# Kernel tuning notes

Measured on AMD Instinct MI355X. Metric: run time of the kernel, lower is better.

Reference implementation:

```python
import jax, jax.numpy as jnp
import numpy as np

B, T, D, U = 2, 512, 768, 768


def setup_inputs() -> dict:
    key = jax.random.key(0)
    kx, kv, ku, kw = jax.random.split(key, 4)
    x = jax.random.normal(kx, (B, T, D), dtype=jnp.float32)
    # glorot-ish scaled params
    V_a = jax.random.normal(kv, (U,), dtype=jnp.float32) * (1.0 / np.sqrt(U))
    U_a = jax.random.normal(ku, (D, U), dtype=jnp.float32) * (1.0 / np.sqrt(D))
    b_u = jnp.zeros((U,), dtype=jnp.float32)
    W_a = jax.random.normal(kw, (D, U), dtype=jnp.float32) * (1.0 / np.sqrt(D))
    return {"x": x, "V_a": V_a, "U_a": U_a, "b_u": b_u, "W_a": W_a}


def reference(x, V_a, U_a, b_u, W_a):
    # Bahdanau additive self-attention, fully batched (replaces the per-timestep loop).
    # wx[b,i,u] = x[b,i] @ W_a  (query projection; original recomputed this per step)
    wx = jnp.einsum('bid,du->biu', x, W_a)
    # ux[b,j,u] = x[b,j] @ U_a + b_u  (the _uxpb term)
    ux = jnp.einsum('bjd,du->bju', x, U_a) + b_u
    # e[b,i,j] = V_a . tanh(wx[b,i] + ux[b,j])
    e = jnp.einsum('biju,u->bij', jnp.tanh(wx[:, :, None, :] + ux[:, None, :, :]), V_a)
    # original: exp / sum over keys == softmax over axis j (no mask path)
    at = jax.nn.softmax(e, axis=2)
    # context[b,i,d] = sum_j at[b,i,j] * x[b,j,d]
    return jnp.einsum('bij,bjd->bid', at, x)
```

## Files before the change

### kernel.cpp

```cpp
#include <hip/hip_runtime.h>
#include <hip/hip_bf16.h>

#define BB 2
#define TT 512
#define DD 768
#define UU 768
#define NR (BB*TT)
#define CC 2.8853900817779268f

typedef __attribute__((ext_vector_type(8))) short short8v;
typedef __attribute__((ext_vector_type(4))) float float4v;
typedef __attribute__((ext_vector_type(4))) unsigned short ushort4v;

static __device__ __forceinline__ float fexp2(float x) { return __builtin_amdgcn_exp2f(x); }
static __device__ __forceinline__ float frcp(float x)  { return __builtin_amdgcn_rcpf(x); }
static __device__ __forceinline__ float readlane_f(float v, int l) {
    return __builtin_bit_cast(float, __builtin_amdgcn_readlane(__builtin_bit_cast(unsigned, v), l));
}
static __device__ __forceinline__ unsigned short bf16rn(float f) {
    unsigned u = __builtin_bit_cast(unsigned, f);
    u += 0x7FFFu + ((u >> 16) & 1u);
    return (unsigned short)(u >> 16);
}
static __device__ __forceinline__ float bf16tof(unsigned short h) {
    return __builtin_bit_cast(float, ((unsigned)h) << 16);
}

__global__ __launch_bounds__(256) void prep_split(
    const float* __restrict__ x,
    const float* __restrict__ Wm,
    const float* __restrict__ Um,
    unsigned short* __restrict__ xhi, unsigned short* __restrict__ xlo,
    unsigned short* __restrict__ WThi, unsigned short* __restrict__ WTlo,
    unsigned short* __restrict__ UThi, unsigned short* __restrict__ UTlo)
{
    const int mode = blockIdx.z;
    const int t = threadIdx.x;

    if (mode == 2) {
        const int blk = blockIdx.y * 12 + blockIdx.x;
        const float4* src = (const float4*)x + (size_t)blk * 1024;
        #pragma unroll
        for (int i = 0; i < 4; ++i) {
            const int idx = i * 256 + t;
            const float4 v = src[idx];
            ushort4v h, l;
            h.x = bf16rn(v.x); l.x = bf16rn(v.x - bf16tof(h.x));
            h.y = bf16rn(v.y); l.y = bf16rn(v.y - bf16tof(h.y));
            h.z = bf16rn(v.z); l.z = bf16rn(v.z - bf16tof(h.z));
            h.w = bf16rn(v.w); l.w = bf16rn(v.w - bf16tof(h.w));
            const size_t off = (size_t)blk * 4096 + (size_t)idx * 4;
            *(ushort4v*)(xhi + off) = h;
            *(ushort4v*)(xlo + off) = l;
        }
        return;
    }
    if (blockIdx.y >= 12) return;

    const float* __restrict__ S = (mode == 0) ? Wm : Um;
    unsigned short* __restrict__ Thi = (mode == 0) ? WThi : UThi;
    unsigned short* __restrict__ Tlo = (mode == 0) ? WTlo : UTlo;

    __shared__ float tile[64][65];
    const int d0 = blockIdx.y * 64;
    const int u0 = blockIdx.x * 64;

    #pragma unroll
    for (int i = 0; i < 4; ++i) {
        const int f4 = i * 256 + t;
        const int r  = f4 >> 4;
        const int c4 = f4 & 15;
        const float4 v = *(const float4*)(S + (size_t)(d0 + r) * UU + u0 + c4 * 4);
        tile[r][c4 * 4 + 0] = v.x;
        tile[r][c4 * 4 + 1] = v.y;
        tile[r][c4 * 4 + 2] = v.z;
        tile[r][c4 * 4 + 3] = v.w;
    }
    __syncthreads();
    #pragma unroll
    for (int i = 0; i < 2; ++i) {
        const int cid = i * 256 + t;
        const int ur  = cid >> 3;
        const int kc  = cid & 7;
        short8v H, L;
        #pragma unroll
        for (int j = 0; j < 8; ++j) {
            const float f = tile[kc * 8 + j][ur];
            const unsigned short h = bf16rn(f);
            H[j] = (short)h;
            L[j] = (short)bf16rn(f - bf16tof(h));
        }
        const size_t off = (size_t)(u0 + ur) * DD + d0 + kc * 8;
        *(short8v*)(Thi + off) = H;
        *(short8v*)(Tlo + off) = L;
    }
}

__global__ __launch_bounds__(256) void gemm_mfma(
    const unsigned short* __restrict__ xhi, const unsigned short* __restrict__ xlo,
    const unsigned short* __restrict__ WThi, const unsigned short* __restrict__ WTlo,
    const unsigned short* __restrict__ UThi, const unsigned short* __restrict__ UTlo,
    const float* __restrict__ bu,
    float* __restrict__ EW4,
    float* __restrict__ EUT)
{
    const int mode = blockIdx.z;
    const unsigned short* __restrict__ Ahi = mode ? UThi : WThi;
    const unsigned short* __restrict__ Alo = mode ? UTlo : WTlo;

    __shared__ unsigned short lds[4 * 4096];

    const int tid  = threadIdx.x;
    const int lane = tid & 63;
    const int wid  = tid >> 6;
    const int wm   = wid >> 1, wn = wid & 1;
    const int u0   = blockIdx.y * 64;
    const int r0t  = blockIdx.x * 64;

    const int srow0 = tid >> 3;
    const int srow1 = srow0 + 32;
    const int sc0   = tid & 7;
    const int sw0   = (sc0 ^ (srow0 & 7)) << 3;

    short8v g0, g1, g2, g3, g4, g5, g6, g7;

#define LOADSTEP(K0) { \
    const size_t ka = (size_t)(K0) + sc0 * 8; \
    g0 = *(const short8v*)(Ahi + (size_t)(u0 + srow0) * DD + ka); \
    g1 = *(const short8v*)(Ahi + (size_t)(u0 + srow1) * DD + ka); \
    g2 = *(const short8v*)(Alo + (size_t)(u0 + srow0) * DD + ka); \
    g3 = *(const short8v*)(Alo + (size_t)(u0 + srow1) * DD + ka); \
    g4 = *(const short8v*)(xhi + (size_t)(r0t + srow0) * DD + ka); \
    g5 = *(const short8v*)(xhi + (size_t)(r0t + srow1) * DD + ka); \
    g6 = *(const short8v*)(xlo + (size_t)(r0t + srow0) * DD + ka); \
    g7 = *(const short8v*)(xlo + (size_t)(r0t + srow1) * DD + ka); }

#define WRITESTEP { \
    *(short8v*)&lds[0 * 4096 + srow0 * 64 + sw0] = g0; \
    *(short8v*)&lds[0 * 4096 + srow1 * 64 + sw0] = g1; \
    *(short8v*)&lds[1 * 4096 + srow0 * 64 + sw0] = g2; \
    *(short8v*)&lds[1 * 4096 + srow1 * 64 + sw0] = g3; \
    *(short8v*)&lds[2 * 4096 + srow0 * 64 + sw0] = g4; \
    *(short8v*)&lds[2 * 4096 + srow1 * 64 + sw0] = g5; \
    *(short8v*)&lds[3 * 4096 + srow0 * 64 + sw0] = g6; \
    *(short8v*)&lds[3 * 4096 + srow1 * 64 + sw0] = g7; }

    float4v acc[2][2] = {};

    LOADSTEP(0);
    for (int s = 0; s < 12; ++s) {
        __syncthreads();
        WRITESTEP;
        __syncthreads();
        if (s < 11) LOADSTEP((s + 1) * 64);

        short8v ah[2][2], al[2][2], bh[2][2], bl[2][2];
        #pragma unroll
        for (int f = 0; f < 2; ++f) {
            const int arow = wm * 32 + f * 16 + (lane & 15);
            const int brow = wn * 32 + f * 16 + (lane & 15);
            #pragma unroll
            for (int kk = 0; kk < 2; ++kk) {
                const int ck = kk * 4 + (lane >> 4);
                ah[f][kk] = *(const short8v*)&lds[0 * 4096 + arow * 64 + (((ck ^ (arow & 7))) << 3)];
                al[f][kk] = *(const short8v*)&lds[1 * 4096 + arow * 64 + (((ck ^ (arow & 7))) << 3)];
                bh[f][kk] = *(const short8v*)&lds[2 * 4096 + brow * 64 + (((ck ^ (brow & 7))) << 3)];
                bl[f][kk] = *(const short8v*)&lds[3 * 4096 + brow * 64 + (((ck ^ (brow & 7))) << 3)];
            }
        }
        #pragma unroll
        for (int kk = 0; kk < 2; ++kk)
            #pragma unroll
            for (int m = 0; m < 2; ++m)
                #pragma unroll
                for (int n = 0; n < 2; ++n) {
                    acc[m][n] = __builtin_amdgcn_mfma_f32_16x16x32_bf16(ah[m][kk], bh[n][kk], acc[m][n], 0, 0, 0);
                    acc[m][n] = __builtin_amdgcn_mfma_f32_16x16x32_bf16(ah[m][kk], bl[n][kk], acc[m][n], 0, 0, 0);
                    acc[m][n] = __builtin_amdgcn_mfma_f32_16x16x32_bf16(al[m][kk], bh[n][kk], acc[m][n], 0, 0, 0);
                }
    }

    #pragma unroll
    for (int m = 0; m < 2; ++m) {
        #pragma unroll
        for (int n = 0; n < 2; ++n) {
            const int ub = u0 + wm * 32 + m * 16 + ((lane >> 4) << 2);
            const int r  = r0t + wn * 32 + n * 16 + (lane & 15);
            if (mode == 0) {
                float* dst = EW4 + ((size_t)(r >> 2) * UU + ub) * 4 + (r & 3);
                #pragma unroll
                for (int reg = 0; reg < 4; ++reg)
                    dst[reg * 4] = fexp2(acc[m][n][reg] * CC);
            } else {
                const int b = r >> 9, j = r & 511;
                const float4 bv = *(const float4*)(bu + ub);
                float4v o;
                o[0] = fexp2((acc[m][n][0] + bv.x) * CC);
                o[1] = fexp2((acc[m][n][1] + bv.y) * CC);
                o[2] = fexp2((acc[m][n][2] + bv.z) * CC);
                o[3] = fexp2((acc[m][n][3] + bv.w) * CC);
                *(float4v*)(EUT + (size_t)b * (UU * TT) + (size_t)(ub >> 2) * (TT * 4) + j * 4) = o;
            }
        }
    }
#undef LOADSTEP
#undef WRITESTEP
}

__global__ __launch_bounds__(512) void attn_fused(
    const float* __restrict__ x,
    const float* __restrict__ V_a,
    const float* __restrict__ EW4,
    const float* __restrict__ EUT,
    float* __restrict__ out)
{
    extern __shared__ float smem[];
    float*  part = smem;
    float*  red  = smem;
    float4* sw4  = (float4*)(smem + 12288);
    float*  vv   = smem + 12288 + 3072;

    const int tid  = threadIdx.x;
    const int lane = tid & 63;
    const int w    = tid >> 6;

    const int bid = blockIdx.x;
    const int blk = (bid & 7) * 32 + (bid >> 3);

    const int r0 = blk * 4;
    const int b  = r0 >> 9;

    {
        const float4* __restrict__ ew4q = (const float4*)EW4 + (size_t)blk * UU;
        for (int t = tid; t < UU; t += 512) {
            sw4[t] = ew4q[t];
            vv[t]  = V_a[t];
        }
    }
    __syncthreads();

    const float4* __restrict__ eq = (const float4*)(EUT + (size_t)b * UU * TT) + tid;

    float acc0 = 0.f, acc1 = 0.f, acc2 = 0.f, acc3 = 0.f;

#define PAIR(E0, E1, u0) { \
    const float4 S0 = sw4[(u0)]; \
    const float4 S1 = sw4[(u0) + 1]; \
    const float v0 = vv[(u0)], v1 = vv[(u0) + 1]; \
    { const float da = fmaf((E0), S0.x, 1.f), db = fmaf((E1), S1.x, 1.f); \
      float n = v0 * db; n = fmaf(v1, da, n); \
      acc0 = fmaf(n, frcp(da * db), acc0); } \
    { const float da = fmaf((E0), S0.y, 1.f), db = fmaf((E1), S1.y, 1.f); \
      float n = v0 * db; n = fmaf(v1, da, n); \
      acc1 = fmaf(n, frcp(da * db), acc1); } \
    { const float da = fmaf((E0), S0.z, 1.f), db = fmaf((E1), S1.z, 1.f); \
      float n = v0 * db; n = fmaf(v1, da, n); \
      acc2 = fmaf(n, frcp(da * db), acc2); } \
    { const float da = fmaf((E0), S0.w, 1.f), db = fmaf((E1), S1.w, 1.f); \
      float n = v0 * db; n = fmaf(v1, da, n); \
      acc3 = fmaf(n, frcp(da * db), acc3); } }
#define QUAD(E4, UB) { PAIR((E4).x, (E4).y, (UB)); PAIR((E4).z, (E4).w, (UB)+2); }

    float4 c0 = eq[0 * 512], c1 = eq[1 * 512], c2 = eq[2 * 512], c3 = eq[3 * 512];
    #pragma unroll 1
    for (int c = 0; c < 47; ++c) {
        const int q = 4 * c;
        float4 n0_ = eq[(size_t)(q + 4) * 512];
        float4 n1_ = eq[(size_t)(q + 5) * 512];
        float4 n2_ = eq[(size_t)(q + 6) * 512];
        float4 n3_ = eq[(size_t)(q + 7) * 512];
        const int ub = 16 * c;
        QUAD(c0, ub); QUAD(c1, ub + 4); QUAD(c2, ub + 8); QUAD(c3, ub + 12);
        c0 = n0_; c1 = n1_; c2 = n2_; c3 = n3_;
    }
    QUAD(c0, 752); QUAD(c1, 756); QUAD(c2, 760); QUAD(c3, 764);

    float m0 = acc0, m1 = acc1, m2 = acc2, m3 = acc3;
    #pragma unroll
    for (int off = 32; off; off >>= 1) {
        m0 = fminf(m0, __shfl_xor(m0, off, 64));
        m1 = fminf(m1, __shfl_xor(m1, off, 64));
        m2 = fminf(m2, __shfl_xor(m2, off, 64));
        m3 = fminf(m3, __shfl_xor(m3, off, 64));
    }
    if (lane == 0) {
        red[0 * 8 + w] = m0; red[1 * 8 + w] = m1;
        red[2 * 8 + w] = m2; red[3 * 8 + w] = m3;
    }
    __syncthreads();
    float M0 = red[0], M1 = red[8], M2 = red[16], M3 = red[24];
    #pragma unroll
    for (int k = 1; k < 8; ++k) {
        M0 = fminf(M0, red[0 * 8 + k]);
        M1 = fminf(M1, red[1 * 8 + k]);
        M2 = fminf(M2, red[2 * 8 + k]);
        M3 = fminf(M3, red[3 * 8 + k]);
    }

    const float p0 = fexp2(CC * (M0 - acc0));
    const float p1 = fexp2(CC * (M1 - acc1));
    const float p2 = fexp2(CC * (M2 - acc2));
    const float p3 = fexp2(CC * (M3 - acc3));
    float s0 = p0, s1 = p1, s2 = p2, s3 = p3;
    #pragma unroll
    for (int off = 32; off; off >>= 1) {
        s0 += __shfl_xor(s0, off, 64);
        s1 += __shfl_xor(s1, off, 64);
        s2 += __shfl_xor(s2, off, 64);
        s3 += __shfl_xor(s3, off, 64);
    }
    __syncthreads();
    if (lane == 0) {
        red[32 + 0 * 8 + w] = s0; red[32 + 1 * 8 + w] = s1;
        red[32 + 2 * 8 + w] = s2; red[32 + 3 * 8 + w] = s3;
    }
    __syncthreads();
    float S0 = red[32], S1 = red[40], S2 = red[48], S3 = red[56];
    #pragma unroll
    for (int k = 1; k < 8; ++k) {
        S0 += red[32 + k];
        S1 += red[40 + k];
        S2 += red[48 + k];
        S3 += red[56 + k];
    }
    const float i0 = frcp(S0), i1 = frcp(S1), i2 = frcp(S2), i3 = frcp(S3);

    const float* __restrict__ xb = x + (size_t)b * TT * DD + (size_t)w * 64 * DD + 4 * lane;
    float4 z4 = {0.f, 0.f, 0.f, 0.f};
    float4 pc00 = z4, pc01 = z4, pc02 = z4;
    float4 pc10 = z4, pc11 = z4, pc12 = z4;
    float4 pc20 = z4, pc21 = z4, pc22 = z4;
    float4 pc30 = z4, pc31 = z4, pc32 = z4;

#define F4(dst, a, xv) { dst.x = fmaf(a, xv.x, dst.x); dst.y = fmaf(a, xv.y, dst.y); \
                         dst.z = fmaf(a, xv.z, dst.z); dst.w = fmaf(a, xv.w, dst.w); }
    #pragma unroll 2
    for (int jj = 0; jj < 64; ++jj) {
        const float a0 = readlane_f(p0, jj);
        const float a1 = readlane_f(p1, jj);
        const float a2 = readlane_f(p2, jj);
        const float a3 = readlane_f(p3, jj);
        const float* xr = xb + (size_t)jj * DD;
        const float4 x0 = *(const float4*)(xr);
        const float4 x1 = *(const float4*)(xr + 256);
        const float4 x2 = *(const float4*)(xr + 512);
        F4(pc00, a0, x0); F4(pc01, a0, x1); F4(pc02, a0, x2);
        F4(pc10, a1, x0); F4(pc11, a1, x1); F4(pc12, a1, x2);
        F4(pc20, a2, x0); F4(pc21, a2, x1); F4(pc22, a2, x2);
        F4(pc30, a3, x0); F4(pc31, a3, x1); F4(pc32, a3, x2);
    }

    __syncthreads();
    {
        float* pw = part + w * 1536 + 4 * lane;
        *(float4*)(pw + 0)    = pc00;
        *(float4*)(pw + 256)  = pc01;
        *(float4*)(pw + 512)  = pc02;
        *(float4*)(pw + 768)  = pc10;
        *(float4*)(pw + 1024) = pc11;
        *(float4*)(pw + 1280) = pc12;
    }
    __syncthreads();
    #pragma unroll
    for (int e = 0; e < 3; ++e) {
        const int idx = e * 512 + tid;
        const int r   = (idx >= 768) ? 1 : 0;
        const int d   = idx - r * 768;
        float ssum = 0.f;
        #pragma unroll
        for (int w2 = 0; w2 < 8; ++w2) ssum += part[w2 * 1536 + r * 768 + d];
        out[(size_t)(r0 + r) * DD + d] = ssum * (r ? i1 : i0);
    }
    __syncthreads();
    {
        float* pw = part + w * 1536 + 4 * lane;
        *(float4*)(pw + 0)    = pc20;
        *(float4*)(pw + 256)  = pc21;
        *(float4*)(pw + 512)  = pc22;
        *(float4*)(pw + 768)  = pc30;
        *(float4*)(pw + 1024) = pc31;
        *(float4*)(pw + 1280) = pc32;
    }
    __syncthreads();
    #pragma unroll
    for (int e = 0; e < 3; ++e) {
        const int idx = e * 512 + tid;
        const int r   = (idx >= 768) ? 1 : 0;
        const int d   = idx - r * 768;
        float ssum = 0.f;
        #pragma unroll
        for (int w2 = 0; w2 < 8; ++w2) ssum += part[w2 * 1536 + r * 768 + d];
        out[(size_t)(r0 + 2 + r) * DD + d] = ssum * (r ? i3 : i2);
    }
}

extern "C" void kernel_launch(void* const* d_in, const int* in_sizes, int n_in,
                              void* d_out, int out_size, void* d_ws, size_t ws_size,
                              hipStream_t stream)
{
    const float* x   = (const float*)d_in[0];
    const float* V_a = (const float*)d_in[1];
    const float* U_a = (const float*)d_in[2];
    const float* b_u = (const float*)d_in[3];
    const float* W_a = (const float*)d_in[4];
    float* out = (float*)d_out;

    float* EW4 = (float*)d_ws;
    float* EUT = EW4 + (size_t)UU * NR;
    unsigned short* xhi  = (unsigned short*)(EUT + (size_t)BB * UU * TT);
    unsigned short* xlo  = xhi + (size_t)NR * DD;
    unsigned short* WThi = xlo + (size_t)NR * DD;
    unsigned short* WTlo = WThi + (size_t)UU * DD;
    unsigned short* UThi = WTlo + (size_t)UU * DD;
    unsigned short* UTlo = UThi + (size_t)UU * DD;

    hipLaunchKernelGGL(prep_split, dim3(12, 16, 3), dim3(256), 0, stream,
                       x, W_a, U_a, xhi, xlo, WThi, WTlo, UThi, UTlo);

    hipLaunchKernelGGL(gemm_mfma, dim3(16, 12, 2), dim3(256), 0, stream,
                       xhi, xlo, WThi, WTlo, UThi, UTlo, b_u, EW4, EUT);

    const int ldsB = (12288 + 3072 + 768) * sizeof(float);
    hipLaunchKernelGGL(attn_fused, dim3(NR / 4), dim3(512), ldsB, stream,
                       x, V_a, EW4, EUT, out);
}
```

Baseline: 81.93 us.

## Store key exponentials as fp16 half-exponent and split attention over 1024 threads

New measurement: 84.75 us. 3.5% more time.

```diff
diff --git a/kernel.cpp b/kernel.cpp
--- a/kernel.cpp
+++ b/kernel.cpp
@@ -7,16 +7,15 @@
 #define UU 768
 #define NR (BB*TT)
 #define CC 2.8853900817779268f
+#define HC 1.4426950408889634f
 
 typedef __attribute__((ext_vector_type(8))) short short8v;
 typedef __attribute__((ext_vector_type(4))) float float4v;
 typedef __attribute__((ext_vector_type(4))) unsigned short ushort4v;
+typedef _Float16 half4v __attribute__((ext_vector_type(4)));
 
 static __device__ __forceinline__ float fexp2(float x) { return __builtin_amdgcn_exp2f(x); }
 static __device__ __forceinline__ float frcp(float x)  { return __builtin_amdgcn_rcpf(x); }
-static __device__ __forceinline__ float readlane_f(float v, int l) {
-    return __builtin_bit_cast(float, __builtin_amdgcn_readlane(__builtin_bit_cast(unsigned, v), l));
-}
 static __device__ __forceinline__ unsigned short bf16rn(float f) {
     unsigned u = __builtin_bit_cast(unsigned, f);
     u += 0x7FFFu + ((u >> 16) & 1u);
@@ -102,7 +101,7 @@
     const unsigned short* __restrict__ UThi, const unsigned short* __restrict__ UTlo,
     const float* __restrict__ bu,
     float* __restrict__ EW4,
-    float* __restrict__ EUT)
+    _Float16* __restrict__ EUTH)
 {
     const int mode = blockIdx.z;
     const unsigned short* __restrict__ Ahi = mode ? UThi : WThi;
@@ -194,12 +193,12 @@
             } else {
                 const int b = r >> 9, j = r & 511;
                 const float4 bv = *(const float4*)(bu + ub);
-                float4v o;
-                o[0] = fexp2((acc[m][n][0] + bv.x) * CC);
-                o[1] = fexp2((acc[m][n][1] + bv.y) * CC);
-                o[2] = fexp2((acc[m][n][2] + bv.z) * CC);
-                o[3] = fexp2((acc[m][n][3] + bv.w) * CC);
-                *(float4v*)(EUT + (size_t)b * (UU * TT) + (size_t)(ub >> 2) * (TT * 4) + j * 4) = o;
+                half4v o;
+                o[0] = (_Float16)fexp2((acc[m][n][0] + bv.x) * HC);
+                o[1] = (_Float16)fexp2((acc[m][n][1] + bv.y) * HC);
+                o[2] = (_Float16)fexp2((acc[m][n][2] + bv.z) * HC);
+                o[3] = (_Float16)fexp2((acc[m][n][3] + bv.w) * HC);
+                *(half4v*)(EUTH + ((size_t)(b * 192 + (ub >> 2)) * 512 + j) * 4) = o;
             }
         }
     }
@@ -207,22 +206,26 @@
 #undef WRITESTEP
 }
 
-__global__ __launch_bounds__(512) void attn_fused(
+__global__ __launch_bounds__(1024) void attn_fused(
     const float* __restrict__ x,
     const float* __restrict__ V_a,
     const float* __restrict__ EW4,
-    const float* __restrict__ EUT,
+    const _Float16* __restrict__ EUTH,
     float* __restrict__ out)
 {
     extern __shared__ float smem[];
+    float4* sw4  = (float4*)smem;
+    float*  vv   = smem + 3072;
+    float*  xchg = smem + 4096;
+    float*  red  = smem + 6144;
+    float4* at4  = (float4*)(smem + 8192);
     float*  part = smem;
-    float*  red  = smem;
-    float4* sw4  = (float4*)(smem + 12288);
-    float*  vv   = smem + 12288 + 3072;
+    float*  iv   = smem + 12352;
 
     const int tid  = threadIdx.x;
     const int lane = tid & 63;
-    const int w    = tid >> 6;
+    const int j    = tid & 511;
+    const int uh   = tid >> 9;
 
     const int bid = blockIdx.x;
     const int blk = (bid & 7) * 32 + (bid >> 3);
@@ -230,16 +233,14 @@
     const int r0 = blk * 4;
     const int b  = r0 >> 9;
 
-    {
-        const float4* __restrict__ ew4q = (const float4*)EW4 + (size_t)blk * UU;
-        for (int t = tid; t < UU; t += 512) {
-            sw4[t] = ew4q[t];
-            vv[t]  = V_a[t];
-        }
-    }
-    __syncthreads();
-
-    const float4* __restrict__ eq = (const float4*)(EUT + (size_t)b * UU * TT) + tid;
+    if (tid < UU) {
+        sw4[tid] = ((const float4*)EW4)[(size_t)blk * UU + tid];
+        vv[tid]  = V_a[tid];
+    }
+    __syncthreads();
+
+    const half4v* __restrict__ eqh =
+        (const half4v*)EUTH + (size_t)(b * 192 + uh * 96) * 512 + j;
 
     float acc0 = 0.f, acc1 = 0.f, acc2 = 0.f, acc3 = 0.f;
 
@@ -259,21 +260,35 @@
     { const float da = fmaf((E0), S0.w, 1.f), db = fmaf((E1), S1.w, 1.f); \
       float n = v0 * db; n = fmaf(v1, da, n); \
       acc3 = fmaf(n, frcp(da * db), acc3); } }
-#define QUAD(E4, UB) { PAIR((E4).x, (E4).y, (UB)); PAIR((E4).z, (E4).w, (UB)+2); }
-
-    float4 c0 = eq[0 * 512], c1 = eq[1 * 512], c2 = eq[2 * 512], c3 = eq[3 * 512];
+#define QUADH(H, UB) { \
+    const float e0 = (float)(H)[0], e1 = (float)(H)[1]; \
+    const float e2 = (float)(H)[2], e3 = (float)(H)[3]; \
+    PAIR(e0 * e0, e1 * e1, (UB)); PAIR(e2 * e2, e3 * e3, (UB) + 2); }
+
+    const int ubase = uh * 384 / 4;
+    const int ub0 = uh * 384;
+
+    half4v c0 = eqh[0 * 512], c1 = eqh[1 * 512], c2 = eqh[2 * 512], c3 = eqh[3 * 512];
     #pragma unroll 1
-    for (int c = 0; c < 47; ++c) {
+    for (int c = 0; c < 23; ++c) {
         const int q = 4 * c;
-        float4 n0_ = eq[(size_t)(q + 4) * 512];
-        float4 n1_ = eq[(size_t)(q + 5) * 512];
-        float4 n2_ = eq[(size_t)(q + 6) * 512];
-        float4 n3_ = eq[(size_t)(q + 7) * 512];
-        const int ub = 16 * c;
-        QUAD(c0, ub); QUAD(c1, ub + 4); QUAD(c2, ub + 8); QUAD(c3, ub + 12);
-        c0 = n0_; c1 = n1_; c2 = n2_; c3 = n3_;
-    }
-    QUAD(c0, 752); QUAD(c1, 756); QUAD(c2, 760); QUAD(c3, 764);
+        half4v n0 = eqh[(size_t)(q + 4) * 512];
+        half4v n1 = eqh[(size_t)(q + 5) * 512];
+        half4v n2 = eqh[(size_t)(q + 6) * 512];
+        half4v n3 = eqh[(size_t)(q + 7) * 512];
+        const int ub = ub0 + 16 * c;
+        QUADH(c0, ub); QUADH(c1, ub + 4); QUADH(c2, ub + 8); QUADH(c3, ub + 12);
+        c0 = n0; c1 = n1; c2 = n2; c3 = n3;
+    }
+    QUADH(c0, ub0 + 368); QUADH(c1, ub0 + 372); QUADH(c2, ub0 + 376); QUADH(c3, ub0 + 380);
+    (void)ubase;
+
+    if (uh) *(float4*)&xchg[j * 4] = make_float4(acc0, acc1, acc2, acc3);
+    __syncthreads();
+    if (!uh) {
+        const float4 o = *(float4*)&xchg[j * 4];
+        acc0 += o.x; acc1 += o.y; acc2 += o.z; acc3 += o.w;
+    }
 
     float m0 = acc0, m1 = acc1, m2 = acc2, m3 = acc3;
     #pragma unroll
@@ -283,7 +298,8 @@
         m2 = fminf(m2, __shfl_xor(m2, off, 64));
         m3 = fminf(m3, __shfl_xor(m3, off, 64));
     }
-    if (lane == 0) {
+    if (tid < 512 && lane == 0) {
+        const int w = tid >> 6;
         red[0 * 8 + w] = m0; red[1 * 8 + w] = m1;
         red[2 * 8 + w] = m2; red[3 * 8 + w] = m3;
     }
@@ -310,22 +326,27 @@
         s3 += __shfl_xor(s3, off, 64);
     }
     __syncthreads();
-    if (lane == 0) {
+    if (tid < 512 && lane == 0) {
+        const int w = tid >> 6;
         red[32 + 0 * 8 + w] = s0; red[32 + 1 * 8 + w] = s1;
         red[32 + 2 * 8 + w] = s2; red[32 + 3 * 8 + w] = s3;
     }
     __syncthreads();
-    float S0 = red[32], S1 = red[40], S2 = red[48], S3 = red[56];
-    #pragma unroll
-    for (int k = 1; k < 8; ++k) {
-        S0 += red[32 + k];
-        S1 += red[40 + k];
-        S2 += red[48 + k];
-        S3 += red[56 + k];
-    }
-    const float i0 = frcp(S0), i1 = frcp(S1), i2 = frcp(S2), i3 = frcp(S3);
-
-    const float* __restrict__ xb = x + (size_t)b * TT * DD + (size_t)w * 64 * DD + 4 * lane;
+    if (tid == 0) {
+        float S0 = red[32], S1 = red[40], S2 = red[48], S3 = red[56];
+        #pragma unroll
+        for (int k = 1; k < 8; ++k) {
+            S0 += red[32 + k]; S1 += red[40 + k];
+            S2 += red[48 + k]; S3 += red[56 + k];
+        }
+        iv[0] = frcp(S0); iv[1] = frcp(S1); iv[2] = frcp(S2); iv[3] = frcp(S3);
+    }
+    if (tid < 512) at4[j] = make_float4(p0, p1, p2, p3);
+    __syncthreads();
+
+    const int w16 = tid >> 6;
+    const int jw  = w16 * 32;
+    const float* __restrict__ xb = x + (size_t)b * TT * DD + (size_t)jw * DD + 4 * lane;
     float4 z4 = {0.f, 0.f, 0.f, 0.f};
     float4 pc00 = z4, pc01 = z4, pc02 = z4;
     float4 pc10 = z4, pc11 = z4, pc12 = z4;
@@ -335,63 +356,36 @@
 #define F4(dst, a, xv) { dst.x = fmaf(a, xv.x, dst.x); dst.y = fmaf(a, xv.y, dst.y); \
                          dst.z = fmaf(a, xv.z, dst.z); dst.w = fmaf(a, xv.w, dst.w); }
     #pragma unroll 2
-    for (int jj = 0; jj < 64; ++jj) {
-        const float a0 = readlane_f(p0, jj);
-        const float a1 = readlane_f(p1, jj);
-        const float a2 = readlane_f(p2, jj);
-        const float a3 = readlane_f(p3, jj);
+    for (int jj = 0; jj < 32; ++jj) {
+        const float4 a = at4[jw + jj];
         const float* xr = xb + (size_t)jj * DD;
         const float4 x0 = *(const float4*)(xr);
         const float4 x1 = *(const float4*)(xr + 256);
         const float4 x2 = *(const float4*)(xr + 512);
-        F4(pc00, a0, x0); F4(pc01, a0, x1); F4(pc02, a0, x2);
-        F4(pc10, a1, x0); F4(pc11, a1, x1); F4(pc12, a1, x2);
-        F4(pc20, a2, x0); F4(pc21, a2, x1); F4(pc22, a2, x2);
-        F4(pc30, a3, x0); F4(pc31, a3, x1); F4(pc32, a3, x2);
-    }
-
-    __syncthreads();
-    {
-        float* pw = part + w * 1536 + 4 * lane;
-        *(float4*)(pw + 0)    = pc00;
-        *(float4*)(pw + 256)  = pc01;
-        *(float4*)(pw + 512)  = pc02;
-        *(float4*)(pw + 768)  = pc10;
-        *(float4*)(pw + 1024) = pc11;
-        *(float4*)(pw + 1280) = pc12;
-    }
-    __syncthreads();
-    #pragma unroll
-    for (int e = 0; e < 3; ++e) {
-        const int idx = e * 512 + tid;
-        const int r   = (idx >= 768) ? 1 : 0;
-        const int d   = idx - r * 768;
-        float ssum = 0.f;
-        #pragma unroll
-        for (int w2 = 0; w2 < 8; ++w2) ssum += part[w2 * 1536 + r * 768 + d];
-        out[(size_t)(r0 + r) * DD + d] = ssum * (r ? i1 : i0);
-    }
-    __syncthreads();
-    {
-        float* pw = part + w * 1536 + 4 * lane;
-        *(float4*)(pw + 0)    = pc20;
-        *(float4*)(pw + 256)  = pc21;
-        *(float4*)(pw + 512)  = pc22;
-        *(float4*)(pw + 768)  = pc30;
-        *(float4*)(pw + 1024) = pc31;
-        *(float4*)(pw + 1280) = pc32;
-    }
-    __syncthreads();
-    #pragma unroll
-    for (int e = 0; e < 3; ++e) {
-        const int idx = e * 512 + tid;
-        const int r   = (idx >= 768) ? 1 : 0;
-        const int d   = idx - r * 768;
-        float ssum = 0.f;
-        #pragma unroll
-        for (int w2 = 0; w2 < 8; ++w2) ssum += part[w2 * 1536 + r * 768 + d];
-        out[(size_t)(r0 + 2 + r) * DD + d] = ssum * (r ? i3 : i2);
-    }
+        F4(pc00, a.x, x0); F4(pc01, a.x, x1); F4(pc02, a.x, x2);
+        F4(pc10, a.y, x0); F4(pc11, a.y, x1); F4(pc12, a.y, x2);
+        F4(pc20, a.z, x0); F4(pc21, a.z, x1); F4(pc22, a.z, x2);
+        F4(pc30, a.w, x0); F4(pc31, a.w, x1); F4(pc32, a.w, x2);
+    }
+    __syncthreads();
+
+#define REDPASS(PA, PB, PCc, R) { \
+    *(float4*)&part[w16 * 772 + 4 * lane]       = PA; \
+    *(float4*)&part[w16 * 772 + 256 + 4 * lane] = PB; \
+    *(float4*)&part[w16 * 772 + 512 + 4 * lane] = PCc; \
+    __syncthreads(); \
+    if (tid < 768) { \
+        float ssum = 0.f; \
+        _Pragma("unroll") \
+        for (int w2 = 0; w2 < 16; ++w2) ssum += part[w2 * 772 + tid]; \
+        out[(size_t)(r0 + (R)) * DD + tid] = ssum * iv[(R)]; \
+    } \
+    __syncthreads(); }
+
+    REDPASS(pc00, pc01, pc02, 0);
+    REDPASS(pc10, pc11, pc12, 1);
+    REDPASS(pc20, pc21, pc22, 2);
+    REDPASS(pc30, pc31, pc32, 3);
 }
 
 extern "C" void kernel_launch(void* const* d_in, const int* in_sizes, int n_in,
@@ -406,8 +400,8 @@
     float* out = (float*)d_out;
 
     float* EW4 = (float*)d_ws;
-    float* EUT = EW4 + (size_t)UU * NR;
-    unsigned short* xhi  = (unsigned short*)(EUT + (size_t)BB * UU * TT);
+    _Float16* EUTH = (_Float16*)(EW4 + (size_t)UU * NR);
+    unsigned short* xhi  = (unsigned short*)(EUTH + (size_t)BB * UU * TT);
     unsigned short* xlo  = xhi + (size_t)NR * DD;
     unsigned short* WThi = xlo + (size_t)NR * DD;
     unsigned short* WTlo = WThi + (size_t)UU * DD;
@@ -418,9 +412,9 @@
                        x, W_a, U_a, xhi, xlo, WThi, WTlo, UThi, UTlo);
 
     hipLaunchKernelGGL(gemm_mfma, dim3(16, 12, 2), dim3(256), 0, stream,
-                       xhi, xlo, WThi, WTlo, UThi, UTlo, b_u, EW4, EUT);
-
-    const int ldsB = (12288 + 3072 + 768) * sizeof(float);
-    hipLaunchKernelGGL(attn_fused, dim3(NR / 4), dim3(512), ldsB, stream,
-                       x, V_a, EW4, EUT, out);
-}
+                       xhi, xlo, WThi, WTlo, UThi, UTlo, b_u, EW4, EUTH);
+
+    const int ldsB = 12356 * sizeof(float);
+    hipLaunchKernelGGL(attn_fused, dim3(NR / 4), dim3(1024), ldsB, stream,
+                       x, V_a, EW4, EUTH, out);
+}
```
